# Kernel optimization log

Hardware: AMD Instinct MI355X
Metric: run time of the kernel (lower is better)

The kernel has to match this reference:

```python
import jax, jax.numpy as jnp
import numpy as np
import math

B, T, C = 8, 2048, 1024
H = 16
HD = C // H  # 64 head dim; RoPE operates on HD//2 complex pairs


def setup_inputs() -> dict:
    key = jax.random.key(0)
    k1, k2, k3, k4 = jax.random.split(key, 4)
    x = jax.random.normal(k1, (B, T, C), dtype=jnp.float32)
    # RoPE angles theta[t, i] = t * base**(-2i/HD), as in standard precompute_freqs_cis
    inv_freq = 1.0 / (10000.0 ** (jnp.arange(0, HD, 2, dtype=jnp.float32) / HD))
    freqs = jnp.arange(T, dtype=jnp.float32)[:, None] * inv_freq[None, :]  # [T, HD//2]
    W_attn = jax.random.normal(k2, (C, 3 * C), dtype=jnp.float32) * 0.02
    b_attn = jnp.zeros((3 * C,), dtype=jnp.float32)
    W_proj = jax.random.normal(k3, (C, C), dtype=jnp.float32) * 0.02
    b_proj = jnp.zeros((C,), dtype=jnp.float32)
    return {"x": x, "freqs": freqs, "W_attn": W_attn, "b_attn": b_attn,
            "W_proj": W_proj, "b_proj": b_proj}


def _apply_rope(t, cos, sin):
    # t: [B, T, H, HD] -> view as complex pairs on last dim
    tr = t.reshape(*t.shape[:-1], HD // 2, 2)
    t0, t1 = tr[..., 0], tr[..., 1]
    out0 = t0 * cos - t1 * sin
    out1 = t0 * sin + t1 * cos
    return jnp.stack([out0, out1], axis=-1).reshape(t.shape)


def reference(x, freqs, W_attn, b_attn, W_proj, b_proj):
    Bx, Tx, Cx = x.shape
    qkv = x @ W_attn + b_attn                      # [B, T, 3C]
    q, k, v = jnp.split(qkv, 3, axis=2)
    q = q.reshape(Bx, Tx, H, HD)
    k = k.reshape(Bx, Tx, H, HD)
    v = v.reshape(Bx, Tx, H, HD)
    # rotary embedding (freqs broadcast over batch and heads)
    cos = jnp.cos(freqs)[None, :, None, :]        # [1, T, 1, HD//2]
    sin = jnp.sin(freqs)[None, :, None, :]
    q = _apply_rope(q, cos, sin)
    k = _apply_rope(k, cos, sin)
    # [B, H, T, HD]
    q = q.transpose(0, 2, 1, 3)
    k = k.transpose(0, 2, 1, 3)
    v = v.transpose(0, 2, 1, 3)
    scale = 1.0 / math.sqrt(HD)
    scores = jnp.einsum('bhqd,bhkd->bhqk', q, k) * scale
    causal = jnp.tril(jnp.ones((Tx, Tx), dtype=bool))
    scores = jnp.where(causal[None, None], scores, jnp.finfo(scores.dtype).min)
    att = jax.nn.softmax(scores, axis=-1)
    y = jnp.einsum('bhqk,bhkd->bhqd', att, v)     # [B, H, T, HD]
    y = y.transpose(0, 2, 1, 3).reshape(Bx, Tx, Cx)
    y = y @ W_proj + b_proj
    return y
```

## Files before the change

### kernel.cpp

```cpp
#include <hip/hip_runtime.h>

#define B_ 8
#define T_ 2048
#define C_ 1024
#define H_ 16
#define HD_ 64
#define BH_ (B_ * H_)
#define M_ (B_ * T_)

typedef __attribute__((ext_vector_type(8))) short short8;
typedef __attribute__((ext_vector_type(4))) float floatx4;
typedef __attribute__((ext_vector_type(16))) float floatx16;

__device__ __forceinline__ short f2bf(float f) {
  unsigned int u = __float_as_uint(f);
  u += 0x7fffu + ((u >> 16) & 1u);
  return (short)(u >> 16);
}

__device__ __forceinline__ unsigned pk2(float a, float b) {
  return (unsigned)(unsigned short)f2bf(a) | ((unsigned)(unsigned short)f2bf(b) << 16);
}

__device__ __forceinline__ unsigned cvtpk(float a, float b) {
  unsigned r;
  asm("v_cvt_pk_bf16_f32 %0, %1, %2" : "=v"(r) : "v"(a), "v"(b));
  return r;
}

__device__ __forceinline__ float ex2(float x) {
  float r;
  asm("v_exp_f32 %0, %1" : "=v"(r) : "v"(x));
  return r;
}

__device__ __forceinline__ void g2lds16(const void* g, void* l) {
  __builtin_amdgcn_global_load_lds(
      (const __attribute__((address_space(1))) unsigned int*)g,
      (__attribute__((address_space(3))) unsigned int*)l, 16, 0, 0);
}

__global__ void cvt_x_kernel(const float* __restrict__ x, short* __restrict__ xb, int n8) {
  int i = blockIdx.x * 256 + threadIdx.x;
  if (i >= n8) return;
  const float4* p = reinterpret_cast<const float4*>(x) + (size_t)i * 2;
  float4 a = p[0], b = p[1];
  short8 o;
  o[0] = f2bf(a.x); o[1] = f2bf(a.y); o[2] = f2bf(a.z); o[3] = f2bf(a.w);
  o[4] = f2bf(b.x); o[5] = f2bf(b.y); o[6] = f2bf(b.z); o[7] = f2bf(b.w);
  reinterpret_cast<short8*>(xb)[i] = o;
}

__global__ void transpose_w_kernel(const float* __restrict__ W, short* __restrict__ Wt,
                                   int K, int N) {
  __shared__ float tile[64][65];
  const int k0 = blockIdx.y * 64;
  const int n0 = blockIdx.x * 64;
  const int tid = threadIdx.x;
  const int cc = tid & 15, rr = tid >> 4;
#pragma unroll
  for (int p = 0; p < 4; ++p) {
    int r = p * 16 + rr;
    float4 v = *reinterpret_cast<const float4*>(&W[(size_t)(k0 + r) * N + n0 + cc * 4]);
    tile[r][cc * 4 + 0] = v.x; tile[r][cc * 4 + 1] = v.y;
    tile[r][cc * 4 + 2] = v.z; tile[r][cc * 4 + 3] = v.w;
  }
  __syncthreads();
  const int kk8 = tid & 7, nn = tid >> 3;
#pragma unroll
  for (int p = 0; p < 2; ++p) {
    int n = p * 32 + nn;
    short8 o;
#pragma unroll
    for (int j = 0; j < 8; ++j) o[j] = f2bf(tile[kk8 * 8 + j][n]);
    *reinterpret_cast<short8*>(&Wt[(size_t)(n0 + n) * K + k0 + kk8 * 8]) = o;
  }
}

__global__ void trig_kernel(const float* __restrict__ freqs, float2* __restrict__ cs, int n) {
  int i = blockIdx.x * 256 + threadIdx.x;
  if (i < n) {
    float f = freqs[i];
    cs[i] = make_float2(cosf(f), sinf(f));
  }
}

#define WAIT8 asm volatile("s_waitcnt vmcnt(8)" ::: "memory")
#define WAIT4 asm volatile("s_waitcnt vmcnt(4)" ::: "memory")
#define WAIT0 asm volatile("s_waitcnt vmcnt(0)" ::: "memory")

#define GITER(T, CUR, NXT)                                                        \
  {                                                                               \
    const int tbR = ((T) & 3) << 15;                                              \
                                     \
    _Pragma("unroll") for (int i = 0; i < 4; ++i)                                 \
        af1[i] = *reinterpret_cast<const short8*>(ldsb + tbR + aoff[4 + i]);      \
    __builtin_amdgcn_s_setprio(1);                                                \
    _Pragma("unroll") for (int m = 0; m < 4; ++m)                                 \
        _Pragma("unroll") for (int n = 0; n < 4; ++n)                             \
            acc[m][n] = __builtin_amdgcn_mfma_f32_16x16x32_bf16(                  \
                af0[m], CUR[n], acc[m][n], 0, 0, 0);                              \
    __builtin_amdgcn_s_setprio(0);                                                \
    \
    if ((T) + 3 < NT) { stageA((T) + 3); stageB((T) + 3); }                       \
    if ((T) < NT - 3) { WAIT8; }                                                  \
    else if ((T) == NT - 3) { WAIT4; }                                            \
    else if ((T) == NT - 2) { WAIT0; }                                            \
    asm volatile("s_waitcnt lgkmcnt(0)" ::: "memory");                            \
    __builtin_amdgcn_s_barrier();                                                 \
    if ((T) + 1 < NT) {                                                           \
      const int tbN = (((T) + 1) & 3) << 15;                                      \
      _Pragma("unroll") for (int n = 0; n < 4; ++n)                               \
          NXT[n] = *reinterpret_cast<const short8*>(ldsb + tbN + boff[n]);        \
      _Pragma("unroll") for (int i = 0; i < 4; ++i)                               \
          af0[i] = *reinterpret_cast<const short8*>(ldsb + tbN + aoff[i]);        \
    }                                                                             \
    __builtin_amdgcn_s_setprio(1);                                                \
    _Pragma("unroll") for (int m = 0; m < 4; ++m)                                 \
        _Pragma("unroll") for (int n = 0; n < 4; ++n)                             \
            acc[4 + m][n] = __builtin_amdgcn_mfma_f32_16x16x32_bf16(              \
                af1[m], CUR[n], acc[4 + m][n], 0, 0, 0);                          \
    __builtin_amdgcn_s_setprio(0);                                                \
  }

template <int EPI>
__global__ __launch_bounds__(512, 2) void gemm8_kernel(
    const short* __restrict__ A, const short* __restrict__ Bt,
    const float* __restrict__ bias, int Ndim, int nbx, float* __restrict__ outF,
    short* __restrict__ Qw, short* __restrict__ Kw, short* __restrict__ Vw,
    const float2* __restrict__ trig) {
  constexpr int Kd = 1024, NT = 32;
  __shared__ short lds[65536];
  const char* ldsb = reinterpret_cast<const char*>(lds);
  const int tid = threadIdx.x, l = tid & 63, w = tid >> 6;
  const int wr = w >> 2, wc = w & 3;

  const int nwg = gridDim.x, qq = nwg >> 3;
  const int bid = blockIdx.x;
  const int wg = (bid & 7) * qq + (bid >> 3);
  const int bx = wg % nbx, by = wg / nbx;
  const int m0 = by * 256, n0 = bx * 256;

  const int sup1 = tid >> 3;
  const int lcS = (tid & 7) ^ (sup1 & 7);
  const int rowS = 2 * sup1 + (lcS >> 2);
  const int colS = (lcS & 3) << 3;

  const int cl = l & 15, r4h = l >> 4;
  const int supL = cl >> 1;
  const int aslot = (((cl & 1) << 2) + r4h) ^ supL;
  int aoff[8], boff[4];
#pragma unroll
  for (int m = 0; m < 8; ++m)
    aoff[m] = (wr * 64 + m * 8 + supL) * 128 + aslot * 16;
#pragma unroll
  for (int n = 0; n < 4; ++n)
    boff[n] = 16384 + (wc * 32 + n * 8 + supL) * 128 + aslot * 16;

  auto stageA = [&](int t) {
    const int sb = (t & 3) << 15;
    const int k0 = t * 32;
    g2lds16(&A[(size_t)(m0 + rowS) * Kd + k0 + colS], (char*)lds + sb + tid * 16);
    g2lds16(&A[(size_t)(m0 + rowS + 128) * Kd + k0 + colS],
            (char*)lds + sb + 8192 + tid * 16);
  };
  auto stageB = [&](int t) {
    const int sb = ((t & 3) << 15) + 16384;
    const int k0 = t * 32;
    g2lds16(&Bt[(size_t)(n0 + rowS) * Kd + k0 + colS], (char*)lds + sb + tid * 16);
    g2lds16(&Bt[(size_t)(n0 + rowS + 128) * Kd + k0 + colS],
            (char*)lds + sb + 8192 + tid * 16);
  };

  floatx4 acc[8][4] = {};
  short8 af0[4], af1[4], bbA[4], bbB[4];

  stageA(0); stageB(0);
  stageA(1); stageB(1);
  stageA(2); stageB(2);
  WAIT8;
  __builtin_amdgcn_s_barrier();
#pragma unroll
  for (int n = 0; n < 4; ++n)
    bbA[n] = *reinterpret_cast<const short8*>(ldsb + boff[n]);
#pragma unroll
  for (int i = 0; i < 4; ++i)
    af0[i] = *reinterpret_cast<const short8*>(ldsb + aoff[i]);

  for (int t = 0; t < NT; t += 2) {
    GITER(t, bbA, bbB);
    GITER(t + 1, bbB, bbA);
  }

  const int r4 = r4h * 4;
  if (EPI == 0 && n0 >= 2048) {
    short* vr = &lds[w * 8192];
    const int hh = ((n0 - 2048) >> 6) + wc;
    const int bhv = (m0 >> 11) * 16 + hh;
    const int t0g = (m0 & 2047) + wr * 128;
#pragma unroll
    for (int m = 0; m < 8; ++m) {
#pragma unroll
      for (int n = 0; n < 4; ++n) {
        const int gn = n0 + wc * 64 + n * 16 + cl;
        const float bs = bias[gn];
        const int d = n * 16 + cl;
        const int sW = m * 2 + (r4h >> 1);
        const int byte = d * 256 + (((sW ^ (d & 15))) << 4) + ((r4h & 1) << 3);
        uint2 pv;
        pv.x = cvtpk(acc[m][n][0] + bs, acc[m][n][1] + bs);
        pv.y = cvtpk(acc[m][n][2] + bs, acc[m][n][3] + bs);
        *reinterpret_cast<uint2*>(reinterpret_cast<char*>(vr) + byte) = pv;
      }
    }
#pragma unroll
    for (int g = 0; g < 16; ++g) {
      const int d = g * 4 + r4h;
      const int byte = d * 256 + (((cl ^ (d & 15))) << 4);
      short8 vv = *reinterpret_cast<const short8*>(
          reinterpret_cast<const char*>(vr) + byte);
      *reinterpret_cast<short8*>(&Vw[((size_t)bhv * 64 + d) * 2048 + t0g + cl * 8]) = vv;
    }
  } else {
#pragma unroll
    for (int m = 0; m < 8; ++m) {
#pragma unroll
      for (int n = 0; n < 4; ++n) {
        const int gn = n0 + wc * 64 + n * 16 + cl;
#pragma unroll
        for (int r = 0; r < 4; ++r) {
          const int gm = m0 + wr * 128 + m * 16 + r4 + r;
          float v = acc[m][n][r] + bias[gn];
          if (EPI == 1) {
            outF[(size_t)gm * Ndim + gn] = v;
          } else {
            const int b = gm >> 11, t = gm & 2047;
            const int ccol = gn & 1023;
            const int h = ccol >> 6, d = ccol & 63;
            const int bh = b * 16 + h;
            float2 cs = trig[t * 32 + (d >> 1)];
            float p = __shfl_xor(v, 1);
            float o = (d & 1) ? (p * cs.y + v * cs.x) : (v * cs.x - p * cs.y);
            if ((gn >> 10) == 0) {
              Qw[((size_t)bh * T_ + t) * HD_ + d] = f2bf(o * 0.18033688011112042f);
            } else {
              Kw[((size_t)bh * T_ + t) * HD_ + d] = f2bf(o);
            }
          }
        }
      }
    }
  }
}

__global__ __launch_bounds__(256) void attn_kernel(
    const short* __restrict__ Q, const short* __restrict__ Kw,
    const short* __restrict__ Vt, short* __restrict__ Y) {
  __shared__ short lds[2][4096];
  const int tid = threadIdx.x, l = tid & 63, w = tid >> 6;
  const int ql = l & 31, hi = l >> 5;
  const bool lo32 = (hi == 0);
  const int bh = blockIdx.x;
  const int qb = 15 - (int)blockIdx.y;
  const int q0w = qb * 128 + w * 32;
  const int jlast = 4 * qb + w;
  const int nj = 4 * qb + 4;

  short8 qf[4];
  {
    const size_t qbase = ((size_t)bh * T_ + q0w + ql) * HD_;
#pragma unroll
    for (int s = 0; s < 4; ++s)
      qf[s] = *reinterpret_cast<const short8*>(&Q[qbase + s * 16 + hi * 8]);
  }

  int koffs[4], voffs[4];
#pragma unroll
  for (int s = 0; s < 4; ++s)
    koffs[s] = ql * 64 + (((2 * s + hi) ^ (ql & 7)) * 8);
#pragma unroll
  for (int s2 = 0; s2 < 2; ++s2)
#pragma unroll
    for (int h = 0; h < 2; ++h) {
      int r = 16 * h + (ql >> 1);
      int lc = (ql & 1) * 4 + 2 * s2 + hi;
      voffs[s2 * 2 + h] = r * 64 + ((lc ^ (r & 7)) * 8);
    }

  const int rowSt = tid >> 3, pSt = tid & 7;
  const int gkSt = pSt ^ (rowSt & 7);
  const int dvSt = 2 * rowSt + (gkSt >> 2), kcSt = gkSt & 3;
  const short* kg = &Kw[((size_t)bh * T_ + rowSt) * HD_ + gkSt * 8];
  const short* vg = &Vt[((size_t)bh * HD_ + dvSt) * T_ + kcSt * 8];

  floatx16 o0 = {}, o1 = {};
  float m_run = -1e30f, l_run = 0.f;

#define STAGE_KV(buf)                              \
  {                                                \
    g2lds16(kg, &lds[buf][0] + tid * 8);           \
    g2lds16(vg, &lds[buf][2048] + tid * 8);        \
    kg += 32 * 64;                                 \
    vg += 32;                                      \
  }

  STAGE_KV(0);
  asm volatile("s_waitcnt vmcnt(0)" ::: "memory");
  __syncthreads();

  int cur = 0;
  for (int j = 0; j < nj; ++j) {
    if (j + 1 < nj) STAGE_KV(cur ^ 1);

    if (j <= jlast) {
      const short* bK = &lds[cur][0];
      const short* bV = &lds[cur][2048];
      floatx16 sx = {};
#pragma unroll
      for (int s = 0; s < 4; ++s) {
        short8 ka = *reinterpret_cast<const short8*>(bK + koffs[s]);
        sx = __builtin_amdgcn_mfma_f32_32x32x16_bf16(ka, qf[s], sx, 0, 0, 0);
      }
      if (j == jlast) {
#pragma unroll
        for (int r = 0; r < 16; ++r) {
          int kb = (r & 3) + 8 * (r >> 2) + 4 * hi;
          if (kb > ql) sx[r] = -1e30f;
        }
      }
      float mt = fmaxf(
          fmaxf(fmaxf(fmaxf(sx[0], sx[1]), fmaxf(sx[2], sx[3])),
                fmaxf(fmaxf(sx[4], sx[5]), fmaxf(sx[6], sx[7]))),
          fmaxf(fmaxf(fmaxf(sx[8], sx[9]), fmaxf(sx[10], sx[11])),
                fmaxf(fmaxf(sx[12], sx[13]), fmaxf(sx[14], sx[15]))));
      mt = fmaxf(mt, __shfl_xor(mt, 32));
      if (!__all(mt <= m_run + 8.0f)) {
        float mnew = fmaxf(m_run, mt);
        float sc = ex2(m_run - mnew);
        m_run = mnew;
        l_run *= sc;
#pragma unroll
        for (int r = 0; r < 16; ++r) { o0[r] *= sc; o1[r] *= sc; }
      }
#pragma unroll
      for (int r = 0; r < 16; ++r) sx[r] = ex2(sx[r] - m_run);
      float a0 = (sx[0] + sx[1]) + (sx[2] + sx[3]);
      float a1 = (sx[4] + sx[5]) + (sx[6] + sx[7]);
      float a2 = (sx[8] + sx[9]) + (sx[10] + sx[11]);
      float a3 = (sx[12] + sx[13]) + (sx[14] + sx[15]);
      float sum = (a0 + a1) + (a2 + a3);
      sum += __shfl_xor(sum, 32);
      l_run += sum;
      unsigned pw[8];
#pragma unroll
      for (int i = 0; i < 8; ++i) pw[i] = cvtpk(sx[2 * i], sx[2 * i + 1]);
#pragma unroll
      for (int s2 = 0; s2 < 2; ++s2) {
        unsigned c0 = lo32 ? pw[4 * s2 + 2] : pw[4 * s2];
        unsigned c1 = lo32 ? pw[4 * s2 + 3] : pw[4 * s2 + 1];
        unsigned e0 = __shfl_xor(c0, 32), e1 = __shfl_xor(c1, 32);
        union { unsigned u[4]; short8 s8; } pb;
        pb.u[0] = lo32 ? pw[4 * s2] : e0;
        pb.u[1] = lo32 ? pw[4 * s2 + 1] : e1;
        pb.u[2] = lo32 ? e0 : pw[4 * s2 + 2];
        pb.u[3] = lo32 ? e1 : pw[4 * s2 + 3];
#pragma unroll
        for (int h = 0; h < 2; ++h) {
          short8 va = *reinterpret_cast<const short8*>(bV + voffs[s2 * 2 + h]);
          if (h == 0) o0 = __builtin_amdgcn_mfma_f32_32x32x16_bf16(va, pb.s8, o0, 0, 0, 0);
          else        o1 = __builtin_amdgcn_mfma_f32_32x32x16_bf16(va, pb.s8, o1, 0, 0, 0);
        }
      }
    }
    asm volatile("s_waitcnt vmcnt(0)" ::: "memory");
    __syncthreads();
    cur ^= 1;
  }

  float inv = 1.0f / l_run;
#pragma unroll
  for (int r = 0; r < 16; ++r) { o0[r] *= inv; o1[r] *= inv; }
  __syncthreads();
  short* tb2 = &lds[0][0] + w * 2048;
#pragma unroll
  for (int h = 0; h < 2; ++h) {
#pragma unroll
    for (int qd = 0; qd < 4; ++qd) {
      int dbase = 32 * h + 8 * qd + 4 * hi;
      uint2 v;
      v.x = h == 0 ? cvtpk(o0[4 * qd], o0[4 * qd + 1]) : cvtpk(o1[4 * qd], o1[4 * qd + 1]);
      v.y = h == 0 ? cvtpk(o0[4 * qd + 2], o0[4 * qd + 3]) : cvtpk(o1[4 * qd + 2], o1[4 * qd + 3]);
      int byte = (ql * 128 + dbase * 2) ^ ((ql & 7) << 4);
      *reinterpret_cast<uint2*>(reinterpret_cast<char*>(tb2) + byte) = v;
    }
  }
  const int bb = bh >> 4, hh = bh & 15;
#pragma unroll
  for (int p = 0; p < 4; ++p) {
    int c = p * 64 + l;
    int q = c >> 3, dc = c & 7;
    int byte = (q * 128 + dc * 16) ^ ((q & 7) << 4);
    short8 v = *reinterpret_cast<const short8*>(reinterpret_cast<const char*>(tb2) + byte);
    *reinterpret_cast<short8*>(
        &Y[((size_t)(bb * T_ + q0w + q)) * C_ + hh * 64 + dc * 8]) = v;
  }
#undef STAGE_KV
}

extern "C" void kernel_launch(void* const* d_in, const int* in_sizes, int n_in,
                              void* d_out, int out_size, void* d_ws, size_t ws_size,
                              hipStream_t stream) {
  const float* x      = (const float*)d_in[0];
  const float* freqs  = (const float*)d_in[1];
  const float* W_attn = (const float*)d_in[2];
  const float* b_attn = (const float*)d_in[3];
  const float* W_proj = (const float*)d_in[4];
  const float* b_proj = (const float*)d_in[5];
  float* out = (float*)d_out;
  char* ws = (char*)d_ws;

  const size_t SZ_QKV = (size_t)BH_ * T_ * HD_ * 2;
  short* Qw  = (short*)(ws);
  short* Kw  = (short*)(ws + SZ_QKV);
  short* Vt  = (short*)(ws + 2 * SZ_QKV);
  short* Xb  = (short*)(ws + 3 * SZ_QKV);
  short* WtA = (short*)(ws + 4 * SZ_QKV);
  short* WtP = (short*)(ws + 4 * SZ_QKV + 6291456);
  float2* trig = (float2*)(ws + 4 * SZ_QKV + 6291456 + 2097152);

  cvt_x_kernel<<<(M_ * C_ / 8 + 255) / 256, 256, 0, stream>>>(x, Xb, M_ * C_ / 8);
  transpose_w_kernel<<<dim3(3 * C_ / 64, C_ / 64), 256, 0, stream>>>(W_attn, WtA, C_, 3 * C_);
  transpose_w_kernel<<<dim3(C_ / 64, C_ / 64), 256, 0, stream>>>(W_proj, WtP, C_, C_);
  trig_kernel<<<(T_ * 32 + 255) / 256, 256, 0, stream>>>(freqs, trig, T_ * 32);

  gemm8_kernel<0><<<dim3((3 * C_ / 256) * (M_ / 256)), 512, 0, stream>>>(
      Xb, WtA, b_attn, 3 * C_, 3 * C_ / 256, nullptr, Qw, Kw, Vt, trig);

  attn_kernel<<<dim3(BH_, 16), 256, 0, stream>>>(Qw, Kw, Vt, Xb);

  gemm8_kernel<1><<<dim3((C_ / 256) * (M_ / 256)), 512, 0, stream>>>(
      Xb, WtP, b_proj, C_, C_ / 256, out, nullptr, nullptr, nullptr, nullptr);
}
```

Baseline: 300.0 us.

## Deepen attention KV pipeline to four LDS buffers and use permlane32 swap

The attention kernel moves from a double-buffered K/V stage with a full wait and barrier after every tile to a four-slot ring that keeps three tiles in flight. It waits on partial vmcnt counts and issues one barrier per iteration. The P-operand exchange between lane halves now uses v_permlane32_swap instead of ds_bpermute-style shuffles plus selects. This aims to hide global load latency and cut cross-lane overhead, at the cost of doubling attention LDS (32KB), which may reduce occupancy.

After: 294.0 us. 1.02x faster.

```diff
diff --git a/kernel.cpp b/kernel.cpp
--- a/kernel.cpp
+++ b/kernel.cpp
@@ -16,10 +16,6 @@
   unsigned int u = __float_as_uint(f);
   u += 0x7fffu + ((u >> 16) & 1u);
   return (short)(u >> 16);
-}
-
-__device__ __forceinline__ unsigned pk2(float a, float b) {
-  return (unsigned)(unsigned short)f2bf(a) | ((unsigned)(unsigned short)f2bf(b) << 16);
 }
 
 __device__ __forceinline__ unsigned cvtpk(float a, float b) {
@@ -86,7 +82,9 @@
 }
 
 #define WAIT8 asm volatile("s_waitcnt vmcnt(8)" ::: "memory")
+#define WAIT6 asm volatile("s_waitcnt vmcnt(6)" ::: "memory")
 #define WAIT4 asm volatile("s_waitcnt vmcnt(4)" ::: "memory")
+#define WAIT2 asm volatile("s_waitcnt vmcnt(2)" ::: "memory")
 #define WAIT0 asm volatile("s_waitcnt vmcnt(0)" ::: "memory")
 
 #define GITER(T, CUR, NXT)                                                        \
@@ -256,10 +254,9 @@
 __global__ __launch_bounds__(256) void attn_kernel(
     const short* __restrict__ Q, const short* __restrict__ Kw,
     const short* __restrict__ Vt, short* __restrict__ Y) {
-  __shared__ short lds[2][4096];
+  __shared__ short lds[4][4096];
   const int tid = threadIdx.x, l = tid & 63, w = tid >> 6;
   const int ql = l & 31, hi = l >> 5;
-  const bool lo32 = (hi == 0);
   const int bh = blockIdx.x;
   const int qb = 15 - (int)blockIdx.y;
   const int q0w = qb * 128 + w * 32;
@@ -305,16 +302,19 @@
   }
 
   STAGE_KV(0);
-  asm volatile("s_waitcnt vmcnt(0)" ::: "memory");
-  __syncthreads();
-
-  int cur = 0;
+  STAGE_KV(1);
+  STAGE_KV(2);
+
   for (int j = 0; j < nj; ++j) {
-    if (j + 1 < nj) STAGE_KV(cur ^ 1);
+    if (j < nj - 2) { WAIT4; }
+    else if (j == nj - 2) { WAIT2; }
+    else { WAIT0; }
+    __builtin_amdgcn_s_barrier();
+    if (j + 3 < nj) STAGE_KV((j + 3) & 3);
 
     if (j <= jlast) {
-      const short* bK = &lds[cur][0];
-      const short* bV = &lds[cur][2048];
+      const short* bK = &lds[j & 3][0];
+      const short* bV = &lds[j & 3][2048];
       floatx16 sx = {};
 #pragma unroll
       for (int s = 0; s < 4; ++s) {
@@ -356,14 +356,12 @@
       for (int i = 0; i < 8; ++i) pw[i] = cvtpk(sx[2 * i], sx[2 * i + 1]);
 #pragma unroll
       for (int s2 = 0; s2 < 2; ++s2) {
-        unsigned c0 = lo32 ? pw[4 * s2 + 2] : pw[4 * s2];
-        unsigned c1 = lo32 ? pw[4 * s2 + 3] : pw[4 * s2 + 1];
-        unsigned e0 = __shfl_xor(c0, 32), e1 = __shfl_xor(c1, 32);
+        unsigned a0w = pw[4 * s2 + 0], a1w = pw[4 * s2 + 1];
+        unsigned a2w = pw[4 * s2 + 2], a3w = pw[4 * s2 + 3];
+        asm("v_permlane32_swap_b32 %0, %1" : "+v"(a0w), "+v"(a2w));
+        asm("v_permlane32_swap_b32 %0, %1" : "+v"(a1w), "+v"(a3w));
         union { unsigned u[4]; short8 s8; } pb;
-        pb.u[0] = lo32 ? pw[4 * s2] : e0;
-        pb.u[1] = lo32 ? pw[4 * s2 + 1] : e1;
-        pb.u[2] = lo32 ? e0 : pw[4 * s2 + 2];
-        pb.u[3] = lo32 ? e1 : pw[4 * s2 + 3];
+        pb.u[0] = a0w; pb.u[1] = a1w; pb.u[2] = a2w; pb.u[3] = a3w;
 #pragma unroll
         for (int h = 0; h < 2; ++h) {
           short8 va = *reinterpret_cast<const short8*>(bV + voffs[s2 * 2 + h]);
@@ -372,9 +370,6 @@
         }
       }
     }
-    asm volatile("s_waitcnt vmcnt(0)" ::: "memory");
-    __syncthreads();
-    cur ^= 1;
   }
 
   float inv = 1.0f / l_run;
@@ -394,6 +389,7 @@
       *reinterpret_cast<uint2*>(reinterpret_cast<char*>(tb2) + byte) = v;
     }
   }
+  __syncthreads();
   const int bb = bh >> 4, hh = bh & 15;
 #pragma unroll
   for (int p = 0; p < 4; ++p) {
```
